# Kernel tuning notes

Measured on AMD Instinct MI355X. Metric: run time of the kernel, lower is better.

## Reference

```python
import jax, jax.numpy as jnp
import numpy as np

B, S, D, E, TOPK = 4, 2048, 1024, 8, 2


def setup_inputs() -> dict:
    key = jax.random.key(0)
    k1, k2, k3 = jax.random.split(key, 3)
    scale = 1.0 / np.sqrt(D)
    return {
        "x": jax.random.normal(k1, (B, S, D), dtype=jnp.float32),
        "gate_w": jax.random.normal(k2, (D, E), dtype=jnp.float32) * scale,
        "gate_b": jnp.zeros((E,), dtype=jnp.float32),
        "expert_w": jax.random.normal(k3, (E, D, D), dtype=jnp.float32) * scale,
        "expert_b": jnp.zeros((E, D), dtype=jnp.float32),
        "top_k": TOPK,
    }


def reference(x, gate_w, gate_b, expert_w, expert_b, top_k):
    # Gating: softmax over experts, then top-k expert indices per token.
    logits = x @ gate_w + gate_b                      # [B, S, E]
    probs = jax.nn.softmax(logits, axis=-1)
    _, top_idx = jax.lax.top_k(probs, top_k)          # [B, S, top_k]
    # Binary membership mask (original multiplies by mask, NOT gate probs).
    mask = jax.nn.one_hot(top_idx, probs.shape[-1], dtype=x.dtype).sum(axis=-2)  # [B, S, E]
    # Dense per-expert linear on all tokens (as in the original loop).
    expert_out = jnp.einsum('bsd,edf->bsef', x, expert_w) + expert_b  # [B, S, E, D]
    # Mask-multiply-accumulate over experts.
    return jnp.einsum('bse,bsef->bsf', mask, expert_out)             # [B, S, D]
```

## Files before the change

### kernel.cpp

```cpp
#include <hip/hip_runtime.h>
#include <stdint.h>

#define T_TOK 8192
#define DD    1024
#define EN    8
#define CPAD  16

#define BM 128
#define BN 128
#define BK 32
#define NT (DD / BK)
#define NWG 4096

#define GATE_NB 512

#define AS1 __attribute__((address_space(1)))
#define AS3 __attribute__((address_space(3)))

typedef __bf16 v8bf __attribute__((ext_vector_type(8)));
typedef float  v4f  __attribute__((ext_vector_type(4)));

__device__ __forceinline__ uint16_t f2b(float f) {
  uint32_t u = __builtin_bit_cast(uint32_t, f);
  u += 0x7FFFu + ((u >> 16) & 1u);
  return (uint16_t)(u >> 16);
}
__device__ __forceinline__ float b2f(uint16_t h) {
  uint32_t u = (uint32_t)h << 16;
  return __builtin_bit_cast(float, u);
}

template <bool WRITE_PIDX>
__global__ __launch_bounds__(256) void prep_kernel(
    const float* __restrict__ x, const float* __restrict__ gw,
    const float* __restrict__ gb, uint16_t* __restrict__ xb,
    int* __restrict__ counts, int* __restrict__ lists, int* __restrict__ pidx,
    const float* __restrict__ w, uint16_t* __restrict__ wt) {
  extern __shared__ __align__(16) uint8_t smem[];
  const int bid = blockIdx.x;
  const int tid = threadIdx.x;

  if (bid >= GATE_NB) {
    float (*tile)[65] = (float(*)[65])smem;
    const int tb = bid - GATE_NB;
    const int e = tb >> 8;
    const int rem = tb & 255;
    const int f0 = (rem & 15) * 64, d0 = (rem >> 4) * 64;
    const float* wsrc = w + ((size_t)e << 20);
    uint16_t* wdst = wt + ((size_t)e << 20);
    const int r4 = tid >> 4;
    const int c4 = (tid & 15) * 4;
#pragma unroll
    for (int i = 0; i < 4; ++i) {
      int row = i * 16 + r4;
      const float4 v = *(const float4*)(wsrc + (size_t)(d0 + row) * DD + f0 + c4);
      tile[row][c4 + 0] = v.x; tile[row][c4 + 1] = v.y;
      tile[row][c4 + 2] = v.z; tile[row][c4 + 3] = v.w;
    }
    __syncthreads();
#pragma unroll
    for (int i = 0; i < 4; ++i) {
      int f = i * 16 + r4;
      ushort4 h;
      h.x = f2b(tile[c4 + 0][f]); h.y = f2b(tile[c4 + 1][f]);
      h.z = f2b(tile[c4 + 2][f]); h.w = f2b(tile[c4 + 3][f]);
      *(ushort4*)(wdst + (size_t)(f0 + f) * DD + d0 + c4) = h;
    }
    return;
  }

  float* sgw = (float*)smem;
  float (*sx)[DD] = (float(*)[DD])(smem + 32768);
  int* se1 = (int*)(smem + 49152);
  int* se2 = (int*)(smem + 49152 + 64);
#pragma unroll
  for (int i = 0; i < 32; ++i) sgw[i * 256 + tid] = gw[i * 256 + tid];
  const int t0 = bid * 16;
  const int wid = tid >> 6, lane = tid & 63;
  const int e = lane >> 3, dg = lane & 7;

  for (int r = 0; r < 4; ++r) {
    const int tt = t0 + wid * 4 + r;
    const float4* xg = (const float4*)(x + (size_t)tt * DD);
    float4* sxv = (float4*)sx[wid];
    ushort4* xbv = (ushort4*)(xb + (size_t)tt * DD);
#pragma unroll
    for (int i = 0; i < 4; ++i) {
      float4 v = xg[i * 64 + lane];
      sxv[i * 64 + lane] = v;
      ushort4 h;
      h.x = f2b(v.x); h.y = f2b(v.y); h.z = f2b(v.z); h.w = f2b(v.w);
      xbv[i * 64 + lane] = h;
    }
    __syncthreads();

    const float* xr = sx[wid];
    double a0 = 0.0, a1 = 0.0, a2 = 0.0, a3 = 0.0;
#pragma unroll 8
    for (int k = 0; k < 128; k += 4) {
      int d = dg + k * 8;
      a0 += (double)xr[d]      * (double)sgw[d * 8 + e];
      a1 += (double)xr[d + 8]  * (double)sgw[(d + 8) * 8 + e];
      a2 += (double)xr[d + 16] * (double)sgw[(d + 16) * 8 + e];
      a3 += (double)xr[d + 24] * (double)sgw[(d + 24) * 8 + e];
    }
    double acc = (a0 + a1) + (a2 + a3);
#pragma unroll
    for (int off = 1; off < 8; off <<= 1) acc += __shfl_xor(acc, off);
    acc += (double)gb[e];
    double lg[8];
#pragma unroll
    for (int i = 0; i < 8; ++i) lg[i] = __shfl(acc, i * 8);
    if (lane == 0) {
      int e1 = 0; double m1 = lg[0];
#pragma unroll
      for (int i = 1; i < 8; ++i) if (lg[i] > m1) { m1 = lg[i]; e1 = i; }
      int e2 = 0; double m2 = -1.0e300;
#pragma unroll
      for (int i = 0; i < 8; ++i) if (i != e1 && lg[i] > m2) { m2 = lg[i]; e2 = i; }
      se1[wid * 4 + r] = e1;
      se2[wid * 4 + r] = e2;
    }
    __syncthreads();
  }

  if (tid < EN) {
    int cnt = 0;
#pragma unroll
    for (int i = 0; i < 16; ++i) cnt += (se1[i] == tid) + (se2[i] == tid);
    int base = atomicAdd(&counts[tid * CPAD], cnt);
    int* dst = lists + tid * T_TOK;
    for (int i = 0; i < 16; ++i) {
      if (se1[i] == tid) {
        if (WRITE_PIDX) pidx[2 * (t0 + i)] = tid * T_TOK + base;
        dst[base++] = t0 + i;
      }
      if (se2[i] == tid) {
        if (WRITE_PIDX) pidx[2 * (t0 + i) + 1] = tid * T_TOK + base;
        dst[base++] = t0 + i;
      }
    }
  }
}

template <bool ATOMIC>
__global__ __launch_bounds__(256, 4) void expert_gemm_kernel(
    const uint16_t* __restrict__ xb, const uint16_t* __restrict__ wt,
    const float* __restrict__ eb, const int* __restrict__ counts,
    const int* __restrict__ lists, uint16_t* __restrict__ dst,
    float* __restrict__ dstf) {
  const int orig = blockIdx.x;
  const int e = orig & 7;
  const int rem = orig >> 3;
  const int m0 = (rem >> 3) * BM;
  const int n0 = (rem & 7) * BN;
  const int cnt = counts[e * CPAD];
  if (m0 >= cnt) return;
  int rows = cnt - m0; if (rows > BM) rows = BM;
  int offsE = 0;
  if (!ATOMIC) {
#pragma unroll
    for (int i = 0; i < EN; ++i) offsE += (i < e) ? counts[i * CPAD] : 0;
  }

  __shared__ uint16_t sA[2 * BM * BK];
  __shared__ uint16_t sB[2 * BN * BK];
  __shared__ int toks[BM];

  const int tid = threadIdx.x;
  if (tid < BM) {
    int rr = tid < rows ? tid : 0;
    toks[tid] = lists[e * T_TOK + m0 + rr];
  }
  __syncthreads();

  const int lane = tid & 63;
  const int wid = tid >> 6;
  const int wm = wid >> 1;
  const int wn = wid & 1;

  v4f acc[4][4];
#pragma unroll
  for (int i = 0; i < 4; ++i)
#pragma unroll
    for (int j = 0; j < 4; ++j) acc[i][j] = (v4f){0.f, 0.f, 0.f, 0.f};

  const uint16_t* aptr[2];
  const uint16_t* bptr[2];
  const uint16_t* wte = wt + ((size_t)e << 20) + (size_t)n0 * DD;
#pragma unroll
  for (int i = 0; i < 2; ++i) {
    int idx = i * 256 + tid;
    int row = idx >> 2;
    int koff = (((idx & 3) ^ ((row >> 1) & 3)) << 3);
    aptr[i] = xb + (size_t)toks[row] * DD + koff;
    bptr[i] = wte + (size_t)row * DD + koff;
  }

#define STAGE(buf, k0)                                                          \
  {                                                                             \
    _Pragma("unroll")                                                           \
    for (int i = 0; i < 2; ++i) {                                               \
      int idx = i * 256 + tid;                                                  \
      __builtin_amdgcn_global_load_lds(                                         \
          (const AS1 uint32_t*)(aptr[i] + (k0)),                                \
          (AS3 uint32_t*)(sA + (buf) * (BM * BK) + idx * 8), 16, 0, 0);         \
      __builtin_amdgcn_global_load_lds(                                         \
          (const AS1 uint32_t*)(bptr[i] + (k0)),                                \
          (AS3 uint32_t*)(sB + (buf) * (BN * BK) + idx * 8), 16, 0, 0);         \
    }                                                                           \
  }

  STAGE(0, 0);
  __syncthreads();

  const int c0 = lane >> 4;
  const int rsel = lane & 15;
  int cur = 0;
  for (int kt = 0; kt < NT; ++kt) {
    if (kt + 1 < NT) STAGE(cur ^ 1, (kt + 1) * BK);
    const uint16_t* a_base = sA + cur * (BM * BK);
    const uint16_t* b_base = sB + cur * (BN * BK);
    v8bf af[4], bfr[4];
#pragma unroll
    for (int m = 0; m < 4; ++m) {
      int row_a = wm * 64 + m * 16 + rsel;
      af[m] = *(const v8bf*)(a_base + row_a * BK + ((c0 ^ ((row_a >> 1) & 3)) << 3));
    }
#pragma unroll
    for (int n = 0; n < 4; ++n) {
      int row_b = wn * 64 + n * 16 + rsel;
      bfr[n] = *(const v8bf*)(b_base + row_b * BK + ((c0 ^ ((row_b >> 1) & 3)) << 3));
    }
#pragma unroll
    for (int m = 0; m < 4; ++m)
#pragma unroll
      for (int n = 0; n < 4; ++n)
        acc[m][n] = __builtin_amdgcn_mfma_f32_16x16x32_bf16(
            af[m], bfr[n], acc[m][n], 0, 0, 0);
    __syncthreads();
    cur ^= 1;
  }
#undef STAGE

  const int col = lane & 15, rq = lane >> 4;
  if (!ATOMIC) {
    uint16_t* base = dst + (size_t)(offsE + m0) * DD + n0 + wn * 64 + col;
#pragma unroll
    for (int m = 0; m < 4; ++m) {
#pragma unroll
      for (int j = 0; j < 4; ++j) {
        int trow = wm * 64 + m * 16 + rq * 4 + j;
        if (trow < rows) {
          uint16_t* orow = base + (size_t)trow * DD;
#pragma unroll
          for (int n = 0; n < 4; ++n) orow[n * 16] = f2b(acc[m][n][j]);
        }
      }
    }
  } else {
    float biasv[4];
#pragma unroll
    for (int n = 0; n < 4; ++n)
      biasv[n] = eb[e * DD + n0 + wn * 64 + n * 16 + col];
#pragma unroll
    for (int m = 0; m < 4; ++m) {
#pragma unroll
      for (int j = 0; j < 4; ++j) {
        int trow = wm * 64 + m * 16 + rq * 4 + j;
        if (trow < rows) {
          float* orow = dstf + (size_t)toks[trow] * DD + n0;
#pragma unroll
          for (int n = 0; n < 4; ++n)
            atomicAdd(orow + wn * 64 + n * 16 + col, acc[m][n][j] + biasv[n]);
        }
      }
    }
  }
}

__global__ __launch_bounds__(256) void combine_kernel(
    const uint16_t* __restrict__ wsO, const int* __restrict__ pidx,
    const int* __restrict__ counts, const float* __restrict__ eb,
    float* __restrict__ out) {
  __shared__ int soff[EN];
  const int tid = threadIdx.x;
  if (tid == 0) {
    int o = 0;
#pragma unroll
    for (int i = 0; i < EN; ++i) { soff[i] = o; o += counts[i * CPAD]; }
  }
  __syncthreads();
  const int t0 = blockIdx.x * 4;
#pragma unroll
  for (int r = 0; r < 4; ++r) {
    const int t = t0 + r;
    const int pi1 = pidx[2 * t], pi2 = pidx[2 * t + 1];
    const int e1 = pi1 >> 13, p1 = pi1 & (T_TOK - 1);
    const int e2 = pi2 >> 13, p2 = pi2 & (T_TOK - 1);
    ushort4 r1 = ((const ushort4*)(wsO + (size_t)(soff[e1] + p1) * DD))[tid];
    ushort4 r2 = ((const ushort4*)(wsO + (size_t)(soff[e2] + p2) * DD))[tid];
    v4f b1 = ((const v4f*)(eb + e1 * DD))[tid];
    v4f b2 = ((const v4f*)(eb + e2 * DD))[tid];
    v4f o;
    o[0] = b2f(r1.x) + b2f(r2.x) + b1[0] + b2[0];
    o[1] = b2f(r1.y) + b2f(r2.y) + b1[1] + b2[1];
    o[2] = b2f(r1.z) + b2f(r2.z) + b1[2] + b2[2];
    o[3] = b2f(r1.w) + b2f(r2.w) + b1[3] + b2[3];
    ((v4f*)(out + (size_t)t * DD))[tid] = o;
  }
}

extern "C" void kernel_launch(void* const* d_in, const int* in_sizes, int n_in,
                              void* d_out, int out_size, void* d_ws, size_t ws_size,
                              hipStream_t stream) {
  const float* x  = (const float*)d_in[0];
  const float* gw = (const float*)d_in[1];
  const float* gb = (const float*)d_in[2];
  const float* ew = (const float*)d_in[3];
  const float* ebias = (const float*)d_in[4];
  float* out = (float*)d_out;

  uint8_t* ws = (uint8_t*)d_ws;
  int* counts = (int*)ws;
  int* lists  = (int*)(ws + 512);
  int* pidx   = (int*)(ws + 512 + 262144);
  uint16_t* xb = (uint16_t*)(ws + 512 + 262144 + 65536);
  uint16_t* wt = (uint16_t*)(ws + 512 + 262144 + 65536 + 16777216);
  uint16_t* wsO = (uint16_t*)(ws + 512 + 262144 + 65536 + 2 * 16777216);
  const size_t need = 512ull + 262144 + 65536 + 2 * 16777216 +
                      (size_t)2 * T_TOK * DD * sizeof(uint16_t);
  const bool use_ws = ws_size >= need;

  hipMemsetAsync(counts, 0, 512, stream);
  if (use_ws) {
    prep_kernel<true><<<GATE_NB + 2048, 256, 49408, stream>>>(
        x, gw, gb, xb, counts, lists, pidx, ew, wt);
    expert_gemm_kernel<false><<<NWG, 256, 0, stream>>>(
        xb, wt, ebias, counts, lists, wsO, nullptr);
    combine_kernel<<<T_TOK / 4, 256, 0, stream>>>(wsO, pidx, counts, ebias, out);
  } else {
    hipMemsetAsync(d_out, 0, (size_t)out_size * sizeof(float), stream);
    prep_kernel<false><<<GATE_NB + 2048, 256, 49408, stream>>>(
        x, gw, gb, xb, counts, lists, pidx, ew, wt);
    expert_gemm_kernel<true><<<NWG, 256, 0, stream>>>(
        xb, wt, ebias, counts, lists, nullptr, out);
  }
}
```

Measured before the change: 106.7 us.

## Switch expert GEMM to single-buffered BK=64 tiles with 8-way XOR swizzle

```diff
diff --git a/kernel.cpp b/kernel.cpp
--- a/kernel.cpp
+++ b/kernel.cpp
@@ -8,7 +8,7 @@
 
 #define BM 128
 #define BN 128
-#define BK 32
+#define BK 64
 #define NT (DD / BK)
 #define NWG 4096
 
@@ -163,8 +163,8 @@
     for (int i = 0; i < EN; ++i) offsE += (i < e) ? counts[i * CPAD] : 0;
   }
 
-  __shared__ uint16_t sA[2 * BM * BK];
-  __shared__ uint16_t sB[2 * BN * BK];
+  __shared__ uint16_t sA[BM * BK];
+  __shared__ uint16_t sB[BN * BK];
   __shared__ int toks[BM];
 
   const int tid = threadIdx.x;
@@ -185,63 +185,57 @@
 #pragma unroll
     for (int j = 0; j < 4; ++j) acc[i][j] = (v4f){0.f, 0.f, 0.f, 0.f};
 
-  const uint16_t* aptr[2];
-  const uint16_t* bptr[2];
+  const int koff = (((tid & 7) ^ ((tid >> 3) & 7)) << 3);
   const uint16_t* wte = wt + ((size_t)e << 20) + (size_t)n0 * DD;
-#pragma unroll
-  for (int i = 0; i < 2; ++i) {
-    int idx = i * 256 + tid;
-    int row = idx >> 2;
-    int koff = (((idx & 3) ^ ((row >> 1) & 3)) << 3);
+  const uint16_t* aptr[4];
+  const uint16_t* bptr[4];
+#pragma unroll
+  for (int i = 0; i < 4; ++i) {
+    int row = i * 32 + (tid >> 3);
     aptr[i] = xb + (size_t)toks[row] * DD + koff;
     bptr[i] = wte + (size_t)row * DD + koff;
   }
 
-#define STAGE(buf, k0)                                                          \
-  {                                                                             \
-    _Pragma("unroll")                                                           \
-    for (int i = 0; i < 2; ++i) {                                               \
-      int idx = i * 256 + tid;                                                  \
-      __builtin_amdgcn_global_load_lds(                                         \
-          (const AS1 uint32_t*)(aptr[i] + (k0)),                                \
-          (AS3 uint32_t*)(sA + (buf) * (BM * BK) + idx * 8), 16, 0, 0);         \
-      __builtin_amdgcn_global_load_lds(                                         \
-          (const AS1 uint32_t*)(bptr[i] + (k0)),                                \
-          (AS3 uint32_t*)(sB + (buf) * (BN * BK) + idx * 8), 16, 0, 0);         \
-    }                                                                           \
-  }
-
-  STAGE(0, 0);
-  __syncthreads();
-
   const int c0 = lane >> 4;
   const int rsel = lane & 15;
-  int cur = 0;
+  const int rx = lane & 7;
+
   for (int kt = 0; kt < NT; ++kt) {
-    if (kt + 1 < NT) STAGE(cur ^ 1, (kt + 1) * BK);
-    const uint16_t* a_base = sA + cur * (BM * BK);
-    const uint16_t* b_base = sB + cur * (BN * BK);
-    v8bf af[4], bfr[4];
-#pragma unroll
-    for (int m = 0; m < 4; ++m) {
-      int row_a = wm * 64 + m * 16 + rsel;
-      af[m] = *(const v8bf*)(a_base + row_a * BK + ((c0 ^ ((row_a >> 1) & 3)) << 3));
-    }
-#pragma unroll
-    for (int n = 0; n < 4; ++n) {
-      int row_b = wn * 64 + n * 16 + rsel;
-      bfr[n] = *(const v8bf*)(b_base + row_b * BK + ((c0 ^ ((row_b >> 1) & 3)) << 3));
-    }
-#pragma unroll
-    for (int m = 0; m < 4; ++m)
-#pragma unroll
-      for (int n = 0; n < 4; ++n)
-        acc[m][n] = __builtin_amdgcn_mfma_f32_16x16x32_bf16(
-            af[m], bfr[n], acc[m][n], 0, 0, 0);
-    __syncthreads();
-    cur ^= 1;
-  }
-#undef STAGE
+    const int k0 = kt * BK;
+#pragma unroll
+    for (int i = 0; i < 4; ++i) {
+      int idx = i * 256 + tid;
+      __builtin_amdgcn_global_load_lds(
+          (const AS1 uint32_t*)(aptr[i] + k0),
+          (AS3 uint32_t*)(sA + idx * 8), 16, 0, 0);
+      __builtin_amdgcn_global_load_lds(
+          (const AS1 uint32_t*)(bptr[i] + k0),
+          (AS3 uint32_t*)(sB + idx * 8), 16, 0, 0);
+    }
+    __syncthreads();
+
+#pragma unroll
+    for (int kk = 0; kk < 2; ++kk) {
+      v8bf af[4], bfr[4];
+#pragma unroll
+      for (int m = 0; m < 4; ++m) {
+        int row_a = wm * 64 + m * 16 + rsel;
+        af[m] = *(const v8bf*)(sA + row_a * BK + (((kk * 4 + c0) ^ rx) << 3));
+      }
+#pragma unroll
+      for (int n = 0; n < 4; ++n) {
+        int row_b = wn * 64 + n * 16 + rsel;
+        bfr[n] = *(const v8bf*)(sB + row_b * BK + (((kk * 4 + c0) ^ rx) << 3));
+      }
+#pragma unroll
+      for (int m = 0; m < 4; ++m)
+#pragma unroll
+        for (int n = 0; n < 4; ++n)
+          acc[m][n] = __builtin_amdgcn_mfma_f32_16x16x32_bf16(
+              af[m], bfr[n], acc[m][n], 0, 0, 0);
+    }
+    __syncthreads();
+  }
 
   const int col = lane & 15, rq = lane >> 4;
   if (!ATOMIC) {
```

New measurement: 93.61 us. 1.14x faster.
